# Kernel tuning notes

Hardware: AMD Instinct MI355X
Metric: run time of the kernel (lower is better)

## Reference

```python
import jax, jax.numpy as jnp
import numpy as np

EMBED_DIM = 128
B, SQ, SKV = 16, 2048, 2048


def setup_inputs() -> dict:
    key = jax.random.key(0)
    ks = jax.random.split(key, 8)
    d = EMBED_DIM
    scale = 1.0 / np.sqrt(d)
    return {
        "x": jax.random.normal(ks[0], (B, SQ, d), dtype=jnp.float32),
        "y": jax.random.normal(ks[1], (B, SKV, d), dtype=jnp.float32),
        "Wq": jax.random.normal(ks[2], (d, d), dtype=jnp.float32) * scale,
        "bq": jax.random.normal(ks[3], (d,), dtype=jnp.float32) * 0.02,
        "Wk": jax.random.normal(ks[4], (d, d), dtype=jnp.float32) * scale,
        "bk": jax.random.normal(ks[5], (d,), dtype=jnp.float32) * 0.02,
        "Wv": jax.random.normal(ks[6], (d, d), dtype=jnp.float32) * scale,
        "bv": jax.random.normal(ks[7], (d,), dtype=jnp.float32) * 0.02,
    }


def reference(x, y, Wq, bq, Wk, bk, Wv, bv):
    # Linear projections (torch Linear: x @ W.T + b; here W stored as [in,out])
    q = x @ Wq + bq            # [B, SQ, d]
    k = y @ Wk + bk            # [B, SKV, d]
    v = y @ Wv + bv            # [B, SKV, d]
    # Source scales by q.size(-1)**0.5 = sqrt(embed_dim)
    inv_scale = 1.0 / jnp.sqrt(jnp.asarray(q.shape[-1], q.dtype))
    scores = jnp.einsum("bqd,bkd->bqk", q, k) * inv_scale  # [B, SQ, SKV]
    attn = jax.nn.softmax(scores, axis=-1)
    return jnp.einsum("bqk,bkd->bqd", attn, v)
```

## Files before the change

### kernel.cpp

```cpp
#include <hip/hip_runtime.h>
#include <hip/hip_bf16.h>

typedef unsigned short ushort_t;
typedef __attribute__((ext_vector_type(8))) short short8;
typedef __attribute__((ext_vector_type(4))) float f32x4;
typedef __attribute__((ext_vector_type(16))) float f32x16;

#define MFMA16(a, b, c) __builtin_amdgcn_mfma_f32_16x16x32_bf16((a), (b), (c), 0, 0, 0)
#define MFMA32(a, b, c) __builtin_amdgcn_mfma_f32_32x32x16_bf16((a), (b), (c), 0, 0, 0)

__device__ __forceinline__ ushort_t f2bf(float f) {
    return __builtin_bit_cast(ushort_t, __float2bfloat16(f));
}

#define CVTPK(lo, hi) ({ unsigned int r_; \
    asm("v_cvt_pk_bf16_f32 %0, %1, %2" : "=v"(r_) : "v"(lo), "v"(hi)); r_; })

__device__ __forceinline__ void gl_lds16(const void* g, void* l) {
    __builtin_amdgcn_global_load_lds((const __attribute__((address_space(1))) void*)g,
                                     (__attribute__((address_space(3))) void*)l, 16, 0, 0);
}

__global__ __launch_bounds__(256) void proj3(
    const float* __restrict__ x, const float* __restrict__ y,
    const float* __restrict__ Wq, const float* __restrict__ bq,
    const float* __restrict__ Wk, const float* __restrict__ bk,
    const float* __restrict__ Wv, const float* __restrict__ bv,
    ushort_t* __restrict__ Qd, ushort_t* __restrict__ Kd, ushort_t* __restrict__ VTd,
    float qscale)
{
    __shared__ __align__(16) char smem[65536];

    const int t = threadIdx.x;
    const int mat = blockIdx.x >> 9;
    const int pb  = blockIdx.x & 511;
    const float* src = (mat == 0) ? x : y;
    const float* W   = (mat == 0) ? Wq : (mat == 1) ? Wk : Wv;
    const float* bb  = (mat == 0) ? bq : (mat == 1) ? bk : bv;
    const float  sc  = (mat == 0) ? qscale : 1.0f;

    const int w  = t >> 6;
    const int l  = t & 63;
    const int lg = l >> 4;
    const int ln = l & 15;
    const int acol = lg * 8;

    {
        const char* srcb = (const char*)(src + (size_t)(pb * 64) * 128);
        #pragma unroll
        for (int i = 0; i < 8; ++i) {
            int off = i * 4096 + w * 1024 + l * 16;
            int soff = off ^ (((off >> 9) & 7) << 4);
            gl_lds16(srcb + soff, smem + i * 4096 + w * 1024);
        }
    }

    char* wt = smem + 32768;
    #pragma unroll
    for (int i = 0; i < 16; ++i) {
        int idx = t + i * 256;
        int k  = idx >> 5;
        int c0 = (idx & 31) * 4;
        f32x4 v = ((const f32x4*)W)[idx];
        #pragma unroll
        for (int j = 0; j < 4; ++j) {
            int c = c0 + j;
            int byte = (c * 256 + k * 2) ^ ((c & 7) << 4);
            *(ushort_t*)(wt + byte) = f2bf(v[j]);
        }
    }
    __syncthreads();

    short8 afrag[4];
    {
        const int row = w * 16 + ln;
        const int sw = (row & 7) << 4;
        #pragma unroll
        for (int kc = 0; kc < 4; ++kc) {
            int off0 = row * 512 + lg * 32 + kc * 128;
            f32x4 a0 = *(const f32x4*)(smem + (off0 ^ sw));
            f32x4 a1 = *(const f32x4*)(smem + ((off0 + 16) ^ sw));
            short8 a;
            #pragma unroll
            for (int j = 0; j < 4; ++j) { a[j] = (short)f2bf(a0[j]); a[4 + j] = (short)f2bf(a1[j]); }
            afrag[kc] = a;
        }
    }
    __syncthreads();

    if (mat < 2) {
        ushort_t* tile = (ushort_t*)smem;
        #pragma unroll
        for (int ct = 0; ct < 8; ++ct) {
            f32x4 acc = {0.f, 0.f, 0.f, 0.f};
            const int c = ct * 16 + ln;
            #pragma unroll
            for (int kc = 0; kc < 4; ++kc) {
                int byte = (c * 256 + (kc * 32 + acol) * 2) ^ ((c & 7) << 4);
                short8 bfr = *(const short8*)(wt + byte);
                acc = MFMA16(afrag[kc], bfr, acc);
            }
            float bvv = bb[c];
            #pragma unroll
            for (int reg = 0; reg < 4; ++reg)
                tile[(w * 16 + lg * 4 + reg) * 144 + c] = f2bf((acc[reg] + bvv) * sc);
        }
        __syncthreads();
        const int row = t >> 2, ch = t & 3;
        ushort_t* dst1 = (mat == 0 ? Qd : Kd) + (size_t)(pb * 64 + row) * 128 + ch * 32;
        #pragma unroll
        for (int j = 0; j < 4; ++j)
            *(short8*)(dst1 + j * 8) = *(const short8*)&tile[row * 144 + ch * 32 + j * 8];
    } else {
        ushort_t* vt = (ushort_t*)smem;
        #pragma unroll
        for (int ct = 0; ct < 8; ++ct) {
            f32x4 acc = {0.f, 0.f, 0.f, 0.f};
            const int c = ct * 16 + ln;
            #pragma unroll
            for (int kc = 0; kc < 4; ++kc) {
                int byte = (c * 256 + (kc * 32 + acol) * 2) ^ ((c & 7) << 4);
                short8 bfr = *(const short8*)(wt + byte);
                acc = MFMA16(afrag[kc], bfr, acc);
            }
            float bvv = bb[c];
            #pragma unroll
            for (int reg = 0; reg < 4; ++reg) {
                int rloc = w * 16 + lg * 4 + reg;
                int byte = (c * 128 + rloc * 2) ^ ((c & 7) << 4);
                *(ushort_t*)((char*)vt + byte) = f2bf(acc[reg] + bvv);
            }
        }
        __syncthreads();
        const int r0b = pb * 64;
        const int b   = r0b >> 11;
        const int kv0 = r0b & 2047;
        const int c    = t >> 1;
        const int half = t & 1;
        ushort_t* dst = VTd + (size_t)b * 128 * 2048 + (size_t)c * 2048 + kv0 + half * 32;
        #pragma unroll
        for (int j = 0; j < 4; ++j) {
            int byte = (c * 128 + (half * 32 + j * 8) * 2) ^ ((c & 7) << 4);
            *(short8*)(dst + j * 8) = *(const short8*)((const char*)vt + byte);
        }
    }
}

#define KVBLK 64
#define NT (2048 / KVBLK)
__global__ __launch_bounds__(256) void attn_kernel(
    const ushort_t* __restrict__ Q, const ushort_t* __restrict__ K,
    const ushort_t* __restrict__ VT, float* __restrict__ out)
{
    __shared__ __align__(16) char smem_[65536];

    const int t = threadIdx.x;
    const int bid = (int)blockIdx.x;
    const int wg = (bid & 7) * 64 + (bid >> 3);
    const int b  = wg >> 5;
    const int q0blk = (wg & 31) * 64;

    const char* Kb  = (const char*)(K  + (size_t)b * 2048 * 128);
    const char* VTb = (const char*)(VT + (size_t)b * 128 * 2048);
    const ushort_t* Qb = Q + (size_t)b * 2048 * 128;

    const int w   = t >> 6;
    const int qg  = w >> 1;
    const int kvh = w & 1;
    const int l  = t & 63;
    const int lq = l & 31;
    const int h  = l >> 5;
    const int q0 = q0blk + qg * 32;

    short8 qfrag[8];
    {
        const ushort_t* qp = Qb + (size_t)(q0 + lq) * 128 + h * 8;
        #pragma unroll
        for (int kc = 0; kc < 8; ++kc)
            qfrag[kc] = *(const short8*)(qp + kc * 16);
    }

    f32x16 o[4];
    #pragma unroll
    for (int db = 0; db < 4; ++db)
        #pragma unroll
        for (int i = 0; i < 16; ++i) o[db][i] = 0.f;
    f32x16 ls;
    #pragma unroll
    for (int i = 0; i < 16; ++i) ls[i] = 0.f;

    auto stageK = [&](char* kd, int kt) {
        const char* kb = Kb + (size_t)kt * KVBLK * 256;
        #pragma unroll
        for (int i = 0; i < 4; ++i) {
            int base = w * 4096 + i * 1024;
            int p = base + l * 16;
            int pl = p ^ (((p >> 8) & 15) << 4);
            gl_lds16(kb + pl, kd + base);
        }
    };
    auto stageV = [&](char* vd, int kt) {
        const int kv2 = kt * KVBLK * 2;
        #pragma unroll
        for (int i = 0; i < 4; ++i) {
            int base = w * 4096 + i * 1024;
            int p = base + l * 16;
            int pl = p ^ (((p >> 8) & 15) << 4);
            int dv = ((pl >> 8) << 1) | ((pl >> 7) & 1);
            gl_lds16(VTb + (size_t)dv * 4096 + kv2 + (pl & 127), vd + base);
        }
    };

    stageK(smem_, 0);
    stageV(smem_ + 16384, 0);

    for (int kt = 0; kt < NT; ++kt) {
        const int cur = kt & 1;
        const int ktn = (kt + 1 < NT) ? kt + 1 : 0;
        char* curb = smem_ + cur * 32768;
        char* nxtb = smem_ + (cur ^ 1) * 32768;

        asm volatile("s_waitcnt vmcnt(0)" ::: "memory");
        __builtin_amdgcn_s_barrier();
        stageK(nxtb, ktn);
        stageV(nxtb + 16384, ktn);

        f32x16 s;
        #pragma unroll
        for (int i = 0; i < 16; ++i) s[i] = 0.f;
        const int krow = kvh * 32 + lq;
        const int ksw = (krow & 15) << 4;
        __builtin_amdgcn_s_setprio(1);
        #pragma unroll
        for (int kc = 0; kc < 8; ++kc) {
            int col = (h * 16 + kc * 32) ^ ksw;
            short8 kf = *(const short8*)(curb + krow * 256 + col);
            s = MFMA32(kf, qfrag[kc], s);
        }
        __builtin_amdgcn_s_setprio(0);

        #pragma unroll
        for (int i = 0; i < 16; ++i) s[i] = __builtin_exp2f(s[i]);
        #pragma unroll
        for (int i = 0; i < 16; ++i) ls[i] += s[i];

        short8 pf[2];
        {
            auto pack2 = [&](int a, short8& outf) {
                unsigned u0 = CVTPK(s[a * 8 + 0], s[a * 8 + 1]);
                unsigned u1 = CVTPK(s[a * 8 + 2], s[a * 8 + 3]);
                unsigned u2 = CVTPK(s[a * 8 + 4], s[a * 8 + 5]);
                unsigned u3 = CVTPK(s[a * 8 + 6], s[a * 8 + 7]);
                asm("v_permlane32_swap_b32 %0, %1" : "+v"(u0), "+v"(u2));
                asm("v_permlane32_swap_b32 %0, %1" : "+v"(u1), "+v"(u3));
                union { unsigned wds[4]; short8 s8; } f;
                f.wds[0] = u0; f.wds[1] = u1; f.wds[2] = u2; f.wds[3] = u3;
                outf = f.s8;
            };
            pack2(0, pf[0]);
            pack2(1, pf[1]);
        }

        const char* vlp = curb + 16384;
        __builtin_amdgcn_s_setprio(1);
        #pragma unroll
        for (int db = 0; db < 4; ++db) {
            int d = db * 32 + lq;
            int vrow = d >> 1;
            int vsw = (vrow & 15) << 4;
            #pragma unroll
            for (int ks = 0; ks < 2; ++ks) {
                int colb = ((d & 1) << 7) | (kvh * 64 + ks * 32 + h * 16);
                short8 vf = *(const short8*)(vlp + vrow * 256 + (colb ^ vsw));
                o[db] = MFMA32(vf, pf[ks], o[db]);
            }
        }
        __builtin_amdgcn_s_setprio(0);
    }

    asm volatile("s_waitcnt vmcnt(0)" ::: "memory");

    float lsum;
    {
        float a8[8];
        #pragma unroll
        for (int i = 0; i < 8; ++i) a8[i] = ls[i] + ls[i + 8];
        #pragma unroll
        for (int i = 0; i < 4; ++i) a8[i] += a8[i + 4];
        lsum = (a8[0] + a8[1]) + (a8[2] + a8[3]);
    }
    lsum += __shfl_xor(lsum, 32);

    __syncthreads();
    float* mrg = (float*)smem_;
    const int mo = qg * 4224 + lq * 132;
    const int mlb = 8448;

    if (kvh == 1) {
        #pragma unroll
        for (int db = 0; db < 4; ++db) {
            #pragma unroll
            for (int rq = 0; rq < 4; ++rq) {
                f32x4 v4;
                #pragma unroll
                for (int j = 0; j < 4; ++j) v4[j] = o[db][rq * 4 + j];
                *(f32x4*)&mrg[mo + db * 32 + rq * 8 + 4 * h] = v4;
            }
        }
        if (h == 0) mrg[mlb + qg * 64 + lq] = lsum;
    }
    __syncthreads();
    if (kvh == 0) {
        float inv = 1.0f / (lsum + mrg[mlb + qg * 64 + lq]);
        float* ob = out + (size_t)b * 2048 * 128 + (size_t)(q0 + lq) * 128;
        #pragma unroll
        for (int db = 0; db < 4; ++db) {
            #pragma unroll
            for (int rq = 0; rq < 4; ++rq) {
                f32x4 p4v = *(const f32x4*)&mrg[mo + db * 32 + rq * 8 + 4 * h];
                f32x4 st;
                #pragma unroll
                for (int j = 0; j < 4; ++j)
                    st[j] = (o[db][rq * 4 + j] + p4v[j]) * inv;
                *(f32x4*)(ob + db * 32 + rq * 8 + 4 * h) = st;
            }
        }
    }
}

extern "C" void kernel_launch(void* const* d_in, const int* in_sizes, int n_in,
                              void* d_out, int out_size, void* d_ws, size_t ws_size,
                              hipStream_t stream) {
    (void)in_sizes; (void)n_in; (void)out_size; (void)ws_size;
    const float* x  = (const float*)d_in[0];
    const float* y  = (const float*)d_in[1];
    const float* Wq = (const float*)d_in[2];
    const float* bq = (const float*)d_in[3];
    const float* Wk = (const float*)d_in[4];
    const float* bk = (const float*)d_in[5];
    const float* Wv = (const float*)d_in[6];
    const float* bv = (const float*)d_in[7];
    float* out = (float*)d_out;

    ushort_t* qws  = (ushort_t*)d_ws;
    ushort_t* kws  = qws + (size_t)32768 * 128;
    ushort_t* vtws = kws + (size_t)32768 * 128;

    const float qscale = (float)(1.4426950408889634 / 11.313708498984761);

    proj3<<<1536, 256, 0, stream>>>(x, y, Wq, bq, Wk, bk, Wv, bv, qws, kws, vtws, qscale);
    attn_kernel<<<512, 256, 0, stream>>>(qws, kws, vtws, out);
}
```

Baseline: 94.60 us.

## Software-pipeline attention loop: overlap QK^T of next tile with PV of current

Restructures the KV loop into a two-stage software pipeline. Each step computes the QK^T scores for the next tile and prefetches its V fragments into registers while exp/pack and the PV MFMAs run on the previous tile's scores. The loop is unrolled by two with ping-pong score and V register sets, and launch bounds now request 2 blocks per CU. This aims to hide LDS read latency and softmax ALU time behind MFMA work. The cost is much higher register pressure (two score accumulators plus 16 short8 V fragments), which could cause spills under the occupancy hint.

```diff
diff --git a/kernel.cpp b/kernel.cpp
--- a/kernel.cpp
+++ b/kernel.cpp
@@ -148,7 +148,67 @@
 
 #define KVBLK 64
 #define NT (2048 / KVBLK)
-__global__ __launch_bounds__(256) void attn_kernel(
+
+#define PACK2(S, A, OUTF) {                                          \
+    unsigned u0 = CVTPK(S[(A)*8+0], S[(A)*8+1]);                     \
+    unsigned u1 = CVTPK(S[(A)*8+2], S[(A)*8+3]);                     \
+    unsigned u2 = CVTPK(S[(A)*8+4], S[(A)*8+5]);                     \
+    unsigned u3 = CVTPK(S[(A)*8+6], S[(A)*8+7]);                     \
+    asm("v_permlane32_swap_b32 %0, %1" : "+v"(u0), "+v"(u2));        \
+    asm("v_permlane32_swap_b32 %0, %1" : "+v"(u1), "+v"(u3));        \
+    union { unsigned wds[4]; short8 s8; } f_;                        \
+    f_.wds[0] = u0; f_.wds[1] = u1; f_.wds[2] = u2; f_.wds[3] = u3;  \
+    OUTF = f_.s8;                                                    \
+}
+
+#define STEP(T, SIN, VFIN, SOUT, VFOUT)                                      \
+  {                                                                          \
+    const int ktn_ = ((T) + 2 < NT) ? (T) + 2 : 0;                           \
+    asm volatile("s_waitcnt vmcnt(0)" ::: "memory");                         \
+    __builtin_amdgcn_s_barrier();                                            \
+    char* stb_ = smem_ + (((T) & 1) * 32768);                                \
+    stageK(stb_, ktn_);                                                      \
+    stageV(stb_ + 16384, ktn_);                                              \
+    const char* nb_ = smem_ + ((((T) + 1) & 1) * 32768);                     \
+    _Pragma("unroll")                                                        \
+    for (int i = 0; i < 16; ++i) SOUT[i] = 0.f;                              \
+    __builtin_amdgcn_s_setprio(1);                                           \
+    _Pragma("unroll")                                                        \
+    for (int kc = 0; kc < 8; ++kc) {                                         \
+        int col_ = (h * 16 + kc * 32) ^ ksw;                                 \
+        short8 kf_ = *(const short8*)(nb_ + krow * 256 + col_);              \
+        SOUT = MFMA32(kf_, qfrag[kc], SOUT);                                 \
+    }                                                                        \
+    __builtin_amdgcn_s_setprio(0);                                           \
+    _Pragma("unroll")                                                        \
+    for (int i = 0; i < 16; ++i) SIN[i] = __builtin_exp2f(SIN[i]);           \
+    _Pragma("unroll")                                                        \
+    for (int i = 0; i < 16; ++i) ls[i] += SIN[i];                            \
+    short8 pf0_, pf1_;                                                       \
+    PACK2(SIN, 0, pf0_);                                                     \
+    PACK2(SIN, 1, pf1_);                                                     \
+    __builtin_amdgcn_s_setprio(1);                                           \
+    _Pragma("unroll")                                                        \
+    for (int db = 0; db < 4; ++db) {                                         \
+        o[db] = MFMA32(VFIN[db * 2 + 0], pf0_, o[db]);                       \
+        o[db] = MFMA32(VFIN[db * 2 + 1], pf1_, o[db]);                       \
+    }                                                                        \
+    __builtin_amdgcn_s_setprio(0);                                           \
+    _Pragma("unroll")                                                        \
+    for (int db = 0; db < 4; ++db) {                                         \
+        int d_ = db * 32 + lq;                                               \
+        int vrow_ = d_ >> 1;                                                 \
+        int vsw_ = (vrow_ & 15) << 4;                                        \
+        _Pragma("unroll")                                                    \
+        for (int ks = 0; ks < 2; ++ks) {                                     \
+            int colb_ = ((d_ & 1) << 7) | (kvh * 64 + ks * 32 + h * 16);     \
+            VFOUT[db * 2 + ks] =                                             \
+                *(const short8*)(nb_ + 16384 + vrow_ * 256 + (colb_ ^ vsw_));\
+        }                                                                    \
+    }                                                                        \
+  }
+
+__global__ __launch_bounds__(256, 2) void attn_kernel(
     const ushort_t* __restrict__ Q, const ushort_t* __restrict__ K,
     const ushort_t* __restrict__ VT, float* __restrict__ out)
 {
@@ -211,71 +271,44 @@
         }
     };
 
+    const int krow = kvh * 32 + lq;
+    const int ksw = (krow & 15) << 4;
+
+    f32x16 sA, sB;
+    short8 vfA[8], vfB[8];
+
     stageK(smem_, 0);
     stageV(smem_ + 16384, 0);
-
-    for (int kt = 0; kt < NT; ++kt) {
-        const int cur = kt & 1;
-        const int ktn = (kt + 1 < NT) ? kt + 1 : 0;
-        char* curb = smem_ + cur * 32768;
-        char* nxtb = smem_ + (cur ^ 1) * 32768;
-
-        asm volatile("s_waitcnt vmcnt(0)" ::: "memory");
-        __builtin_amdgcn_s_barrier();
-        stageK(nxtb, ktn);
-        stageV(nxtb + 16384, ktn);
-
-        f32x16 s;
-        #pragma unroll
-        for (int i = 0; i < 16; ++i) s[i] = 0.f;
-        const int krow = kvh * 32 + lq;
-        const int ksw = (krow & 15) << 4;
-        __builtin_amdgcn_s_setprio(1);
-        #pragma unroll
-        for (int kc = 0; kc < 8; ++kc) {
-            int col = (h * 16 + kc * 32) ^ ksw;
-            short8 kf = *(const short8*)(curb + krow * 256 + col);
-            s = MFMA32(kf, qfrag[kc], s);
-        }
-        __builtin_amdgcn_s_setprio(0);
-
-        #pragma unroll
-        for (int i = 0; i < 16; ++i) s[i] = __builtin_exp2f(s[i]);
-        #pragma unroll
-        for (int i = 0; i < 16; ++i) ls[i] += s[i];
-
-        short8 pf[2];
-        {
-            auto pack2 = [&](int a, short8& outf) {
-                unsigned u0 = CVTPK(s[a * 8 + 0], s[a * 8 + 1]);
-                unsigned u1 = CVTPK(s[a * 8 + 2], s[a * 8 + 3]);
-                unsigned u2 = CVTPK(s[a * 8 + 4], s[a * 8 + 5]);
-                unsigned u3 = CVTPK(s[a * 8 + 6], s[a * 8 + 7]);
-                asm("v_permlane32_swap_b32 %0, %1" : "+v"(u0), "+v"(u2));
-                asm("v_permlane32_swap_b32 %0, %1" : "+v"(u1), "+v"(u3));
-                union { unsigned wds[4]; short8 s8; } f;
-                f.wds[0] = u0; f.wds[1] = u1; f.wds[2] = u2; f.wds[3] = u3;
-                outf = f.s8;
-            };
-            pack2(0, pf[0]);
-            pack2(1, pf[1]);
-        }
-
-        const char* vlp = curb + 16384;
-        __builtin_amdgcn_s_setprio(1);
-        #pragma unroll
-        for (int db = 0; db < 4; ++db) {
-            int d = db * 32 + lq;
-            int vrow = d >> 1;
-            int vsw = (vrow & 15) << 4;
-            #pragma unroll
-            for (int ks = 0; ks < 2; ++ks) {
-                int colb = ((d & 1) << 7) | (kvh * 64 + ks * 32 + h * 16);
-                short8 vf = *(const short8*)(vlp + vrow * 256 + (colb ^ vsw));
-                o[db] = MFMA32(vf, pf[ks], o[db]);
-            }
-        }
-        __builtin_amdgcn_s_setprio(0);
+    asm volatile("s_waitcnt vmcnt(0)" ::: "memory");
+    __builtin_amdgcn_s_barrier();
+    stageK(smem_ + 32768, 1);
+    stageV(smem_ + 49152, 1);
+
+    #pragma unroll
+    for (int i = 0; i < 16; ++i) sA[i] = 0.f;
+    __builtin_amdgcn_s_setprio(1);
+    #pragma unroll
+    for (int kc = 0; kc < 8; ++kc) {
+        int col = (h * 16 + kc * 32) ^ ksw;
+        short8 kf = *(const short8*)(smem_ + krow * 256 + col);
+        sA = MFMA32(kf, qfrag[kc], sA);
+    }
+    __builtin_amdgcn_s_setprio(0);
+    #pragma unroll
+    for (int db = 0; db < 4; ++db) {
+        int d = db * 32 + lq;
+        int vrow = d >> 1;
+        int vsw = (vrow & 15) << 4;
+        #pragma unroll
+        for (int ks = 0; ks < 2; ++ks) {
+            int colb = ((d & 1) << 7) | (kvh * 64 + ks * 32 + h * 16);
+            vfA[db * 2 + ks] = *(const short8*)(smem_ + 16384 + vrow * 256 + (colb ^ vsw));
+        }
+    }
+
+    for (int tt = 0; tt < NT; tt += 2) {
+        STEP(tt,     sA, vfA, sB, vfB);
+        STEP(tt + 1, sB, vfB, sA, vfA);
     }
 
     asm volatile("s_waitcnt vmcnt(0)" ::: "memory");
```

After: 92.25 us, median of 4. 1.03x faster.

## Drop KV-split across waves in attention, use 2-wave blocks with 32-wide KV tiles

Applied to the files above, without the earlier changes.

The attention kernel no longer splits each KV tile between two waves that merge partial outputs through LDS at the end. Each block now has two waves, each owning 32 query rows and processing the full KV sequence in 32-row tiles, with half-size double-buffered LDS. This removes the final cross-wave merge and its barriers and lets more blocks fit per CU thanks to the smaller LDS footprint. In exchange it doubles the KV loop iterations and per-tile barriers, and each block has fewer waves to hide load latency.

```diff
diff --git a/kernel.cpp b/kernel.cpp
--- a/kernel.cpp
+++ b/kernel.cpp
@@ -4,6 +4,7 @@
 typedef unsigned short ushort_t;
 typedef __attribute__((ext_vector_type(8))) short short8;
 typedef __attribute__((ext_vector_type(4))) float f32x4;
+typedef __attribute__((ext_vector_type(8))) float f32x8;
 typedef __attribute__((ext_vector_type(16))) float f32x16;
 
 #define MFMA16(a, b, c) __builtin_amdgcn_mfma_f32_16x16x32_bf16((a), (b), (c), 0, 0, 0)
@@ -146,13 +147,13 @@
     }
 }
 
-#define KVBLK 64
+#define KVBLK 32
 #define NT (2048 / KVBLK)
-__global__ __launch_bounds__(256) void attn_kernel(
+__global__ __launch_bounds__(128) void attn_kernel(
     const ushort_t* __restrict__ Q, const ushort_t* __restrict__ K,
     const ushort_t* __restrict__ VT, float* __restrict__ out)
 {
-    __shared__ __align__(16) char smem_[65536];
+    __shared__ __align__(16) char smem_[32768];
 
     const int t = threadIdx.x;
     const int bid = (int)blockIdx.x;
@@ -164,13 +165,11 @@
     const char* VTb = (const char*)(VT + (size_t)b * 128 * 2048);
     const ushort_t* Qb = Q + (size_t)b * 2048 * 128;
 
-    const int w   = t >> 6;
-    const int qg  = w >> 1;
-    const int kvh = w & 1;
+    const int w  = t >> 6;
     const int l  = t & 63;
     const int lq = l & 31;
     const int h  = l >> 5;
-    const int q0 = q0blk + qg * 32;
+    const int q0 = q0blk + w * 32;
 
     short8 qfrag[8];
     {
@@ -185,17 +184,16 @@
     for (int db = 0; db < 4; ++db)
         #pragma unroll
         for (int i = 0; i < 16; ++i) o[db][i] = 0.f;
-    f32x16 ls;
+    f32x8 ls;
     #pragma unroll
-    for (int i = 0; i < 16; ++i) ls[i] = 0.f;
+    for (int i = 0; i < 8; ++i) ls[i] = 0.f;
 
     auto stageK = [&](char* kd, int kt) {
         const char* kb = Kb + (size_t)kt * KVBLK * 256;
         #pragma unroll
         for (int i = 0; i < 4; ++i) {
-            int base = w * 4096 + i * 1024;
-            int p = base + l * 16;
-            int pl = p ^ (((p >> 8) & 15) << 4);
+            int base = i * 2048 + w * 1024 + l * 16;
+            int pl = base ^ (((base >> 8) & 15) << 4);
             gl_lds16(kb + pl, kd + base);
         }
     };
@@ -203,38 +201,37 @@
         const int kv2 = kt * KVBLK * 2;
         #pragma unroll
         for (int i = 0; i < 4; ++i) {
-            int base = w * 4096 + i * 1024;
-            int p = base + l * 16;
-            int pl = p ^ (((p >> 8) & 15) << 4);
-            int dv = ((pl >> 8) << 1) | ((pl >> 7) & 1);
-            gl_lds16(VTb + (size_t)dv * 4096 + kv2 + (pl & 127), vd + base);
+            int base = i * 2048 + w * 1024 + l * 16;
+            int pl = base ^ (((base >> 8) & 15) << 4);
+            int d = ((pl >> 8) << 2) | ((pl >> 6) & 3);
+            gl_lds16(VTb + (size_t)d * 4096 + kv2 + (pl & 63), vd + base);
         }
     };
 
+    const int ksw = (lq & 15) << 4;
+
     stageK(smem_, 0);
-    stageV(smem_ + 16384, 0);
+    stageV(smem_ + 8192, 0);
 
     for (int kt = 0; kt < NT; ++kt) {
         const int cur = kt & 1;
         const int ktn = (kt + 1 < NT) ? kt + 1 : 0;
-        char* curb = smem_ + cur * 32768;
-        char* nxtb = smem_ + (cur ^ 1) * 32768;
+        char* curb = smem_ + cur * 16384;
+        char* nxtb = smem_ + (cur ^ 1) * 16384;
 
         asm volatile("s_waitcnt vmcnt(0)" ::: "memory");
         __builtin_amdgcn_s_barrier();
         stageK(nxtb, ktn);
-        stageV(nxtb + 16384, ktn);
+        stageV(nxtb + 8192, ktn);
 
         f32x16 s;
         #pragma unroll
         for (int i = 0; i < 16; ++i) s[i] = 0.f;
-        const int krow = kvh * 32 + lq;
-        const int ksw = (krow & 15) << 4;
         __builtin_amdgcn_s_setprio(1);
         #pragma unroll
         for (int kc = 0; kc < 8; ++kc) {
             int col = (h * 16 + kc * 32) ^ ksw;
-            short8 kf = *(const short8*)(curb + krow * 256 + col);
+            short8 kf = *(const short8*)(curb + lq * 256 + col);
             s = MFMA32(kf, qfrag[kc], s);
         }
         __builtin_amdgcn_s_setprio(0);
@@ -242,38 +239,42 @@
         #pragma unroll
         for (int i = 0; i < 16; ++i) s[i] = __builtin_exp2f(s[i]);
         #pragma unroll
-        for (int i = 0; i < 16; ++i) ls[i] += s[i];
-
-        short8 pf[2];
+        for (int i = 0; i < 8; ++i) ls[i] += s[i] + s[i + 8];
+
+        short8 pf0, pf1;
         {
-            auto pack2 = [&](int a, short8& outf) {
-                unsigned u0 = CVTPK(s[a * 8 + 0], s[a * 8 + 1]);
-                unsigned u1 = CVTPK(s[a * 8 + 2], s[a * 8 + 3]);
-                unsigned u2 = CVTPK(s[a * 8 + 4], s[a * 8 + 5]);
-                unsigned u3 = CVTPK(s[a * 8 + 6], s[a * 8 + 7]);
-                asm("v_permlane32_swap_b32 %0, %1" : "+v"(u0), "+v"(u2));
-                asm("v_permlane32_swap_b32 %0, %1" : "+v"(u1), "+v"(u3));
-                union { unsigned wds[4]; short8 s8; } f;
-                f.wds[0] = u0; f.wds[1] = u1; f.wds[2] = u2; f.wds[3] = u3;
-                outf = f.s8;
-            };
-            pack2(0, pf[0]);
-            pack2(1, pf[1]);
-        }
-
-        const char* vlp = curb + 16384;
+            unsigned u0 = CVTPK(s[0], s[1]);
+            unsigned u1 = CVTPK(s[2], s[3]);
+            unsigned u2 = CVTPK(s[4], s[5]);
+            unsigned u3 = CVTPK(s[6], s[7]);
+            asm("v_permlane32_swap_b32 %0, %1" : "+v"(u0), "+v"(u2));
+            asm("v_permlane32_swap_b32 %0, %1" : "+v"(u1), "+v"(u3));
+            union { unsigned wds[4]; short8 s8; } f;
+            f.wds[0] = u0; f.wds[1] = u1; f.wds[2] = u2; f.wds[3] = u3;
+            pf0 = f.s8;
+            unsigned v0 = CVTPK(s[8], s[9]);
+            unsigned v1 = CVTPK(s[10], s[11]);
+            unsigned v2 = CVTPK(s[12], s[13]);
+            unsigned v3 = CVTPK(s[14], s[15]);
+            asm("v_permlane32_swap_b32 %0, %1" : "+v"(v0), "+v"(v2));
+            asm("v_permlane32_swap_b32 %0, %1" : "+v"(v1), "+v"(v3));
+            union { unsigned wds[4]; short8 s8; } g;
+            g.wds[0] = v0; g.wds[1] = v1; g.wds[2] = v2; g.wds[3] = v3;
+            pf1 = g.s8;
+        }
+
+        const char* vlp = curb + 8192;
         __builtin_amdgcn_s_setprio(1);
         #pragma unroll
         for (int db = 0; db < 4; ++db) {
             int d = db * 32 + lq;
-            int vrow = d >> 1;
+            int vrow = d >> 2;
             int vsw = (vrow & 15) << 4;
-            #pragma unroll
-            for (int ks = 0; ks < 2; ++ks) {
-                int colb = ((d & 1) << 7) | (kvh * 64 + ks * 32 + h * 16);
-                short8 vf = *(const short8*)(vlp + vrow * 256 + (colb ^ vsw));
-                o[db] = MFMA32(vf, pf[ks], o[db]);
-            }
+            int qd  = (d & 3) * 64;
+            short8 vf0 = *(const short8*)(vlp + vrow * 256 + ((qd + h * 16) ^ vsw));
+            o[db] = MFMA32(vf0, pf0, o[db]);
+            short8 vf1 = *(const short8*)(vlp + vrow * 256 + ((qd + 32 + h * 16) ^ vsw));
+            o[db] = MFMA32(vf1, pf1, o[db]);
         }
         __builtin_amdgcn_s_setprio(0);
     }
@@ -282,48 +283,23 @@
 
     float lsum;
     {
-        float a8[8];
-        #pragma unroll
-        for (int i = 0; i < 8; ++i) a8[i] = ls[i] + ls[i + 8];
-        #pragma unroll
-        for (int i = 0; i < 4; ++i) a8[i] += a8[i + 4];
-        lsum = (a8[0] + a8[1]) + (a8[2] + a8[3]);
+        float a4[4];
+        #pragma unroll
+        for (int i = 0; i < 4; ++i) a4[i] = ls[i] + ls[i + 4];
+        lsum = (a4[0] + a4[1]) + (a4[2] + a4[3]);
     }
     lsum += __shfl_xor(lsum, 32);
 
-    __syncthreads();
-    float* mrg = (float*)smem_;
-    const int mo = qg * 4224 + lq * 132;
-    const int mlb = 8448;
-
-    if (kvh == 1) {
-        #pragma unroll
-        for (int db = 0; db < 4; ++db) {
-            #pragma unroll
-            for (int rq = 0; rq < 4; ++rq) {
-                f32x4 v4;
-                #pragma unroll
-                for (int j = 0; j < 4; ++j) v4[j] = o[db][rq * 4 + j];
-                *(f32x4*)&mrg[mo + db * 32 + rq * 8 + 4 * h] = v4;
-            }
-        }
-        if (h == 0) mrg[mlb + qg * 64 + lq] = lsum;
-    }
-    __syncthreads();
-    if (kvh == 0) {
-        float inv = 1.0f / (lsum + mrg[mlb + qg * 64 + lq]);
-        float* ob = out + (size_t)b * 2048 * 128 + (size_t)(q0 + lq) * 128;
-        #pragma unroll
-        for (int db = 0; db < 4; ++db) {
-            #pragma unroll
-            for (int rq = 0; rq < 4; ++rq) {
-                f32x4 p4v = *(const f32x4*)&mrg[mo + db * 32 + rq * 8 + 4 * h];
-                f32x4 st;
-                #pragma unroll
-                for (int j = 0; j < 4; ++j)
-                    st[j] = (o[db][rq * 4 + j] + p4v[j]) * inv;
-                *(f32x4*)(ob + db * 32 + rq * 8 + 4 * h) = st;
-            }
+    float inv = 1.0f / lsum;
+    float* ob = out + (size_t)b * 2048 * 128 + (size_t)(q0 + lq) * 128;
+    #pragma unroll
+    for (int db = 0; db < 4; ++db) {
+        #pragma unroll
+        for (int rq = 0; rq < 4; ++rq) {
+            f32x4 st;
+            #pragma unroll
+            for (int j = 0; j < 4; ++j) st[j] = o[db][rq * 4 + j] * inv;
+            *(f32x4*)(ob + db * 32 + rq * 8 + 4 * h) = st;
         }
     }
 }
@@ -349,5 +325,5 @@
     const float qscale = (float)(1.4426950408889634 / 11.313708498984761);
 
     proj3<<<1536, 256, 0, stream>>>(x, y, Wq, bq, Wk, bk, Wv, bv, qws, kws, vtws, qscale);
-    attn_kernel<<<512, 256, 0, stream>>>(qws, kws, vtws, out);
-}
+    attn_kernel<<<512, 128, 0, stream>>>(qws, kws, vtws, out);
+}
```

New measurement: 125.1 us. 32.3% more time.
